# Optimization experiments

Hardware: AMD Instinct MI355X
Metric: run time of the kernel (lower is better)

Reference implementation:

```python
import jax
import jax.numpy as jnp
import numpy as np

N_NODES = 4096
N_EDGES = 65536
D_FEAT = 64


def setup_inputs() -> dict:
    key = jax.random.key(0)
    k1, k2, k3, k4 = jax.random.split(key, 4)
    x = jax.random.normal(k1, (N_NODES, D_FEAT), dtype=jnp.float32)
    edge_index = jax.random.randint(k2, (2, N_EDGES), 0, N_NODES, dtype=jnp.int32)
    batch = jnp.zeros((N_NODES,), dtype=jnp.int32)
    # GraphConv(in_channels, 1): lin_rel (with bias) on aggregated neighbors, lin_root on self
    w_rel = jax.random.normal(k3, (D_FEAT, 1), dtype=jnp.float32) * 0.1
    w_root = jax.random.normal(k4, (D_FEAT, 1), dtype=jnp.float32) * 0.1
    b = jnp.zeros((1,), dtype=jnp.float32)
    return {"x": x, "edge_index": edge_index, "batch": batch,
            "w_rel": w_rel, "w_root": w_root, "b": b}


def _merge_stars(x, src0, dst0, score):
    """Faithful sequential greedy star contraction (priority order by score desc)."""
    N = x.shape[0]
    order = jnp.argsort(-score)  # descending, ties like argsort

    def step(carry, node):
        xc, src, dst, remaining, center = carry
        active = remaining[node]
        # dests = set of targets of edges whose (current, rewritten) source == node,
        # minus already-chosen center nodes
        dest_edge = src == node                                  # [E]
        dest_node = jnp.zeros(N, bool).at[dst].max(dest_edge)    # node-level set
        dest_node = dest_node & ~center
        # torch does sum over list(dests)+[node]: node counted again (even on self-loop)
        combine = jnp.einsum('n,nd->d', dest_node.astype(xc.dtype), xc) + xc[node]
        D = dest_node.at[node].set(True)                         # dests U {node}
        x2 = xc.at[node].set(combine)
        src2 = jnp.where(D[src], node, src)                      # np.isin rewrite
        dst2 = jnp.where(D[dst], node, dst)
        rem2 = remaining & ~dest_node
        cen2 = center.at[node].set(True)
        carry2 = (jnp.where(active, x2, xc),
                  jnp.where(active, src2, src),
                  jnp.where(active, dst2, dst),
                  jnp.where(active, rem2, remaining),
                  jnp.where(active, cen2, center))
        return carry2, None

    init = (x, src0, dst0, jnp.ones(N, bool), jnp.zeros(N, bool))
    (x_final, _, _, remaining, _), _ = jax.lax.scan(step, init, order)
    return x_final, remaining


def reference(x, edge_index, batch, w_rel, w_root, b):
    N, d = x.shape
    src0, dst0 = edge_index[0], edge_index[1]
    # GraphConv score: W_rel * sum_{j->i} x_j + b + W_root * x_i ; dropout p=0; tanh
    agg = jax.ops.segment_sum(x[src0], dst0, num_segments=N)     # [N, d]
    score = jnp.tanh((agg @ w_rel + x @ w_root + b).reshape(-1)) # [N]

    x_final, remaining = _merge_stars(x, src0, dst0, score)

    # perm = sorted(nodes_remaining); outputs padded to static size N (sentinel -1)
    perm = jnp.nonzero(remaining, size=N, fill_value=N)[0]
    x_pooled = jnp.take(x_final, perm, axis=0, mode='fill', fill_value=0.0)
    kept = perm < N
    batch_pooled = jnp.where(kept, jnp.take(batch, jnp.minimum(perm, N - 1)), -1)
    # filter_adj on the ORIGINAL edge_index: keep edges with both endpoints kept,
    # relabel nodes to their rank among kept nodes; invalid edges -> -1
    relabel = jnp.cumsum(remaining.astype(jnp.int32)) - 1
    valid = remaining[src0] & remaining[dst0]
    new_src = jnp.where(valid, relabel[src0], -1)
    new_dst = jnp.where(valid, relabel[dst0], -1)
    new_edge_index = jnp.stack([new_src, new_dst])
    perm_out = jnp.where(kept, perm, -1)
    return x_pooled, new_edge_index, batch_pooled, perm_out
```

## Files before the change

### kernel.cpp

```cpp
#include <hip/hip_runtime.h>

#define NN 4096
#define NE 65536
#define ND 64


__global__ void k1_dots_count(const float* __restrict__ x, const float* __restrict__ wrel,
                              const float* __restrict__ wroot, const int* __restrict__ ei,
                              double* __restrict__ srel, double* __restrict__ sroot,
                              int* __restrict__ cnt) {
    int gt = blockIdx.x * blockDim.x + threadIdx.x;
    int node = gt >> 6, lane = gt & 63;
    double xv = (double)x[node * ND + lane];
    double pr = xv * (double)wrel[lane];
    double po = xv * (double)wroot[lane];
    for (int off = 32; off > 0; off >>= 1) {
        pr += __shfl_down(pr, off);
        po += __shfl_down(po, off);
    }
    if (lane == 0) {
        srel[node] = pr;
        sroot[node] = po;
    }
    if (gt < NE / 4) {
        const int4* eid4 = (const int4*)(ei + NE);
        int4 q = eid4[gt];
        atomicAdd(&cnt[q.x], 1);
        atomicAdd(&cnt[q.y], 1);
        atomicAdd(&cnt[q.z], 1);
        atomicAdd(&cnt[q.w], 1);
    }
}

__global__ void __launch_bounds__(1024) k2_scan(const int* __restrict__ cnt,
                                                int* __restrict__ rowst,
                                                int* __restrict__ cursor) {
    __shared__ int wt[16];
    int tid = threadIdx.x, lane = tid & 63, wv = tid >> 6;
    int4 c = ((const int4*)cnt)[tid];
    int tot = c.x + c.y + c.z + c.w;
    int inc = tot;
    for (int off = 1; off < 64; off <<= 1) {
        int v = __shfl_up(inc, off);
        if (lane >= off) inc += v;
    }
    if (lane == 63) wt[wv] = inc;
    __syncthreads();
    if (wv == 0 && lane < 16) {
        int v = wt[lane];
        for (int off = 1; off < 16; off <<= 1) {
            int u2 = __shfl_up(v, off);
            if (lane >= off) v += u2;
        }
        wt[lane] = v;
    }
    __syncthreads();
    int waveoff = (wv > 0) ? wt[wv - 1] : 0;
    int excl = waveoff + inc - tot;
    int4 rs;
    rs.x = excl; rs.y = excl + c.x; rs.z = excl + c.x + c.y; rs.w = excl + c.x + c.y + c.z;
    ((int4*)rowst)[tid] = rs;
    ((int4*)cursor)[tid] = rs;
    if (tid == 0) rowst[NN] = NE;
}

__global__ void k3_scatter(const int* __restrict__ ei, int* __restrict__ cursor,
                           unsigned short* __restrict__ incsr) {
    int i = blockIdx.x * blockDim.x + threadIdx.x;
    const int4* eis4 = (const int4*)ei;
    const int4* eid4 = (const int4*)(ei + NE);
    int4 s = eis4[i];
    int4 d = eid4[i];
    incsr[atomicAdd(&cursor[d.x], 1)] = (unsigned short)s.x;
    incsr[atomicAdd(&cursor[d.y], 1)] = (unsigned short)s.y;
    incsr[atomicAdd(&cursor[d.z], 1)] = (unsigned short)s.z;
    incsr[atomicAdd(&cursor[d.w], 1)] = (unsigned short)s.w;
}

__global__ void k4_keys(const double* __restrict__ srel, const double* __restrict__ sroot,
                        const float* __restrict__ bptr, const int* __restrict__ rowst,
                        const unsigned short* __restrict__ incsr, unsigned* __restrict__ key) {
    int v = blockIdx.x * blockDim.x + threadIdx.x;
    int rs = rowst[v], re = rowst[v + 1];
    double s = 0.0;
    for (int e = rs; e < re; ++e) s += srel[(int)incsr[e]];
    double arg = s + sroot[v] + (double)bptr[0];
    float sc = tanhf((float)arg);
    unsigned m = __float_as_uint(sc);
    m = (m & 0x80000000u) ? ~m : (m | 0x80000000u);
    key[v] = m;
}

__global__ void k5_filtersort(const int* __restrict__ rowst, const unsigned* __restrict__ key,
                              unsigned short* __restrict__ incsr, int* __restrict__ rl) {
    int gt = blockIdx.x * blockDim.x + threadIdx.x;
    int v = gt >> 6, l = gt & 63;
    int rs = rowst[v], deg = rowst[v + 1] - rs;
    unsigned mv = key[v];
    if (deg <= 64) {
        int u = (l < deg) ? (int)incsr[rs + l] : -1;
        bool isself = (l < deg) && (u == v);
        unsigned mu = (l < deg && !isself) ? key[u] : 0u;
        bool keep = (l < deg) && !isself && (mu > mv || (mu == mv && u < v));
        unsigned long long val = keep
            ? ((((unsigned long long)(~mu)) << 12) | (unsigned)u) : ~0ULL;
        int m = __popcll(__ballot(keep));
        bool selfAny = __ballot(isself) != 0ULL;
        for (int k = 2; k <= 64; k <<= 1) {
            for (int j = k >> 1; j > 0; j >>= 1) {
                unsigned long long o = __shfl_xor(val, j);
                bool takeMin = ((l & k) == 0) == ((l & j) == 0);
                unsigned long long mn = (o < val) ? o : val;
                unsigned long long mx = (o < val) ? val : o;
                val = takeMin ? mn : mx;
            }
        }
        if (l < m) incsr[rs + l] = (unsigned short)(val & 0xFFFULL);
        if (l == 0) rl[v] = m | (selfAny ? 0x10000 : 0);
    } else if (l == 0) {
        int w = rs;
        bool selfAny = false;
        for (int e = rs; e < rs + deg; ++e) {
            int u = (int)incsr[e];
            if (u == v) { selfAny = true; continue; }
            unsigned mu = key[u];
            if (!(mu > mv || (mu == mv && u < v))) continue;
            int j = w;
            while (j > rs) {
                int q = (int)incsr[j - 1];
                unsigned mq = key[q];
                if (mu > mq || (mu == mq && u < q)) { incsr[j] = (unsigned short)q; --j; }
                else break;
            }
            incsr[j] = (unsigned short)u; ++w;
        }
        rl[v] = (w - rs) | (selfAny ? 0x10000 : 0);
    }
}

__global__ void __launch_bounds__(1024) k34_fix(
        const int* __restrict__ rowst, const int* __restrict__ rl,
        const unsigned short* __restrict__ incsr_g,
        int* __restrict__ map_g, int* __restrict__ rem_g, int* __restrict__ relab_g,
        int* __restrict__ perm_a, int* __restrict__ nkeep_g) {
    __shared__ __align__(16) char buf[135232];
    unsigned short* incsr = (unsigned short*)buf;
    volatile unsigned char* stat = (volatile unsigned char*)(buf + 131072);
    int* wt = (int*)(buf + 135168);
    int tid = threadIdx.x, lane = tid & 63, wv = tid >> 6;

    for (int i = tid; i < 131072 / 16; i += 1024)
        ((int4*)incsr)[i] = ((const int4*)incsr_g)[i];
    ((int*)(buf + 131072))[tid] = 0;
    int4 rsq = ((const int4*)rowst)[tid];
    int4 rlq = ((const int4*)rl)[tid];
    int rs4[4] = {rsq.x, rsq.y, rsq.z, rsq.w};
    int rq4[4] = {rlq.x, rlq.y, rlq.z, rlq.w};
    __syncthreads();

    unsigned resolved = 0, centerm = 0, selfm = 0;
    int pos4[4], re4[4], fu4[4] = {0, 0, 0, 0};
    #pragma unroll
    for (int t = 0; t < 4; ++t) {
        int v = 4 * tid + t;
        int m = rq4[t] & 0xFFFF;
        if (rq4[t] & 0x10000) selfm |= 1u << t;
        int lo = rs4[t];
        pos4[t] = lo; re4[t] = lo + m;
        if (m == 0) {
            map_g[v] = v; stat[v] = 1;
            centerm |= 1u << t; resolved |= 1u << t;
        } else {
            fu4[t] = (int)incsr[lo];
        }
    }

    int guard = 0;
    while (resolved != 0xFu && guard < 1000000) {
        ++guard;
        bool prog = false;
        #pragma unroll
        for (int t = 0; t < 4; ++t) {
            if (resolved & (1u << t)) continue;
            int v = 4 * tid + t;
            int u = fu4[t];
            int st = (int)stat[u];
            if (st == 0) continue;
            prog = true;
            if (st == 1) {
                map_g[v] = u; stat[v] = 2; resolved |= 1u << t; continue;
            }
            int p = pos4[t] + 1, hi = re4[t];
            bool done = false;
            while (p < hi) {
                u = (int)incsr[p];
                st = (int)stat[u];
                if (st == 2) { ++p; continue; }
                if (st == 1) {
                    map_g[v] = u; stat[v] = 2; resolved |= 1u << t; done = true;
                }
                break;
            }
            if (!done) {
                if (p >= hi) {
                    map_g[v] = v; stat[v] = 1; centerm |= 1u << t; resolved |= 1u << t;
                } else {
                    pos4[t] = p; fu4[t] = u;
                }
            }
        }
        if (__ballot(prog) == 0) __builtin_amdgcn_s_sleep(1);
    }
    __syncthreads();

    int remb[4], cnt4 = 0;
    #pragma unroll
    for (int t = 0; t < 4; ++t) {
        remb[t] = ((centerm >> t) & 1) && !((selfm >> t) & 1);
        cnt4 += remb[t];
    }
    int inc2 = cnt4;
    for (int off = 1; off < 64; off <<= 1) {
        int v = __shfl_up(inc2, off);
        if (lane >= off) inc2 += v;
    }
    if (lane == 63) wt[wv] = inc2;
    __syncthreads();
    if (wv == 0 && lane < 16) {
        int v = wt[lane];
        for (int off = 1; off < 16; off <<= 1) {
            int u2 = __shfl_up(v, off);
            if (lane >= off) v += u2;
        }
        wt[lane] = v;
    }
    __syncthreads();
    int woff2 = (wv > 0) ? wt[wv - 1] : 0;
    int run = woff2 + inc2 - cnt4;
    #pragma unroll
    for (int t = 0; t < 4; ++t) {
        int v = 4 * tid + t;
        relab_g[v] = run;
        if (remb[t]) { perm_a[run] = v; ++run; }
        rem_g[v] = remb[t];
    }
    if (tid == 1023) nkeep_g[0] = run;
}

__global__ void k56_outputs(const float* __restrict__ x, const int* __restrict__ map_g,
                            const int* __restrict__ rem_g, const int* __restrict__ relab_g,
                            const int* __restrict__ perm_a, const int* __restrict__ ei,
                            const int* __restrict__ batch, const int* __restrict__ nkeep_g,
                            float* __restrict__ out) {
    int idx = blockIdx.x * blockDim.x + threadIdx.x;
    if (idx < NN * ND) {
        int n = idx >> 6, d = idx & 63;
        int m = map_g[n];
        if (rem_g[m]) atomicAdd(&out[relab_g[m] * ND + d], x[idx]);
    } else if (idx < NN * ND + 2 * NE) {
        int e = idx - NN * ND;
        int row = e >> 16;
        int ee = e & (NE - 1);
        int s = ei[ee], t = ei[NE + ee];
        bool valid = (rem_g[s] != 0) && (rem_g[t] != 0);
        int endp = (row == 0) ? s : t;
        out[idx] = valid ? (float)relab_g[endp] : -1.0f;
    } else if (idx < NN * ND + 2 * NE + NN) {
        int r = idx - (NN * ND + 2 * NE);
        int nk = nkeep_g[0];
        out[idx] = (r < nk) ? (float)batch[perm_a[r]] : -1.0f;
    } else if (idx < NN * ND + 2 * NE + 2 * NN) {
        int r = idx - (NN * ND + 2 * NE + NN);
        int nk = nkeep_g[0];
        out[idx] = (r < nk) ? (float)perm_a[r] : -1.0f;
    }
}

extern "C" void kernel_launch(void* const* d_in, const int* in_sizes, int n_in,
                              void* d_out, int out_size, void* d_ws, size_t ws_size,
                              hipStream_t stream) {
    const float* x     = (const float*)d_in[0];
    const int*   ei    = (const int*)d_in[1];
    const int*   batch = (const int*)d_in[2];
    const float* wrel  = (const float*)d_in[3];
    const float* wroot = (const float*)d_in[4];
    const float* b     = (const float*)d_in[5];

    char* ws = (char*)d_ws;
    double* srel   = (double*)(ws + 0);
    double* sroot  = (double*)(ws + 32768);
    int*    map_g  = (int*)(ws + 65536);
    int*    rem_g  = (int*)(ws + 81920);
    int*    relab  = (int*)(ws + 98304);
    int*    perma  = (int*)(ws + 114688);
    int*    nkeep  = (int*)(ws + 131072);
    int*    cnt    = (int*)(ws + 131136);
    int*    rowst  = (int*)(ws + 147520);
    int*    cursor = (int*)(ws + 163968);
    unsigned short* incsr = (unsigned short*)(ws + 180352);
    int*      rl  = cnt;
    unsigned* key = (unsigned*)cursor;

    float* out = (float*)d_out;

    hipMemsetAsync(out, 0, NN * ND * sizeof(float), stream);
    hipMemsetAsync(cnt, 0, NN * sizeof(int), stream);
    k1_dots_count<<<NN * ND / 256, 256, 0, stream>>>(x, wrel, wroot, ei, srel, sroot, cnt);
    k2_scan<<<1, 1024, 0, stream>>>(cnt, rowst, cursor);
    k3_scatter<<<(NE / 4) / 256, 256, 0, stream>>>(ei, cursor, incsr);
    k4_keys<<<NN / 256, 256, 0, stream>>>(srel, sroot, b, rowst, incsr, key);
    k5_filtersort<<<(NN * 64) / 256, 256, 0, stream>>>(rowst, key, incsr, rl);
    k34_fix<<<1, 1024, 0, stream>>>(rowst, rl, incsr, map_g, rem_g, relab, perma, nkeep);
    int total_out = NN * ND + 2 * NE + 2 * NN;
    k56_outputs<<<(total_out + 255) / 256, 256, 0, stream>>>(x, map_g, rem_g, relab,
                                                             perma, ei, batch, nkeep, out);
}
```

Baseline: 142.0 us.

## Fuse prefix scan into count kernel via last-block pattern; batch stat loads

```diff
diff --git a/kernel.cpp b/kernel.cpp
--- a/kernel.cpp
+++ b/kernel.cpp
@@ -5,13 +5,16 @@
 #define ND 64
 
 
-__global__ void k1_dots_count(const float* __restrict__ x, const float* __restrict__ wrel,
-                              const float* __restrict__ wroot, const int* __restrict__ ei,
-                              double* __restrict__ srel, double* __restrict__ sroot,
-                              int* __restrict__ cnt) {
+__global__ void k12_dots_count_scan(const float* __restrict__ x,
+                                    const float* __restrict__ wrel,
+                                    const float* __restrict__ wroot,
+                                    const int* __restrict__ ei,
+                                    double* __restrict__ srel, double* __restrict__ sroot,
+                                    int* __restrict__ cnt, int* __restrict__ done,
+                                    int* __restrict__ rowst, int* __restrict__ cursor) {
     int gt = blockIdx.x * blockDim.x + threadIdx.x;
     int node = gt >> 6, lane = gt & 63;
-    double xv = (double)x[node * ND + lane];
+    double xv = (double)x[gt];
     double pr = xv * (double)wrel[lane];
     double po = xv * (double)wroot[lane];
     for (int off = 32; off > 0; off >>= 1) {
@@ -30,38 +33,41 @@
         atomicAdd(&cnt[q.z], 1);
         atomicAdd(&cnt[q.w], 1);
     }
-}
-
-__global__ void __launch_bounds__(1024) k2_scan(const int* __restrict__ cnt,
-                                                int* __restrict__ rowst,
-                                                int* __restrict__ cursor) {
-    __shared__ int wt[16];
-    int tid = threadIdx.x, lane = tid & 63, wv = tid >> 6;
-    int4 c = ((const int4*)cnt)[tid];
-    int tot = c.x + c.y + c.z + c.w;
-    int inc = tot;
+    __threadfence();
+    __syncthreads();
+    __shared__ int isLast;
+    if (threadIdx.x == 0)
+        isLast = (atomicAdd(done, 1) == (int)gridDim.x - 1);
+    __syncthreads();
+    if (!isLast) return;
+
+    int tid = threadIdx.x;
+    int l2 = tid & 63, wv2 = tid >> 6;
+    __shared__ int wt2[4];
+    int vals[16], s = 0;
+    #pragma unroll
+    for (int k = 0; k < 16; ++k) {
+        vals[k] = __hip_atomic_load(&cnt[tid * 16 + k], __ATOMIC_RELAXED,
+                                    __HIP_MEMORY_SCOPE_AGENT);
+        s += vals[k];
+    }
+    int incl = s;
     for (int off = 1; off < 64; off <<= 1) {
-        int v = __shfl_up(inc, off);
-        if (lane >= off) inc += v;
-    }
-    if (lane == 63) wt[wv] = inc;
-    __syncthreads();
-    if (wv == 0 && lane < 16) {
-        int v = wt[lane];
-        for (int off = 1; off < 16; off <<= 1) {
-            int u2 = __shfl_up(v, off);
-            if (lane >= off) v += u2;
-        }
-        wt[lane] = v;
-    }
-    __syncthreads();
-    int waveoff = (wv > 0) ? wt[wv - 1] : 0;
-    int excl = waveoff + inc - tot;
-    int4 rs;
-    rs.x = excl; rs.y = excl + c.x; rs.z = excl + c.x + c.y; rs.w = excl + c.x + c.y + c.z;
-    ((int4*)rowst)[tid] = rs;
-    ((int4*)cursor)[tid] = rs;
-    if (tid == 0) rowst[NN] = NE;
+        int v = __shfl_up(incl, off);
+        if (l2 >= off) incl += v;
+    }
+    if (l2 == 63) wt2[wv2] = incl;
+    __syncthreads();
+    int woff = 0;
+    for (int w = 0; w < wv2; ++w) woff += wt2[w];
+    int run = woff + incl - s;
+    #pragma unroll
+    for (int k = 0; k < 16; ++k) {
+        rowst[tid * 16 + k] = run;
+        cursor[tid * 16 + k] = run;
+        run += vals[k];
+    }
+    if (tid == 255) rowst[NN] = NE;
 }
 
 __global__ void k3_scatter(const int* __restrict__ ei, int* __restrict__ cursor,
@@ -179,13 +185,16 @@
     while (resolved != 0xFu && guard < 1000000) {
         ++guard;
         bool prog = false;
+        int stq[4];
+        #pragma unroll
+        for (int t = 0; t < 4; ++t)
+            stq[t] = (resolved & (1u << t)) ? -1 : (int)stat[fu4[t]];
         #pragma unroll
         for (int t = 0; t < 4; ++t) {
-            if (resolved & (1u << t)) continue;
+            int st = stq[t];
+            if (st <= 0) continue;
             int v = 4 * tid + t;
             int u = fu4[t];
-            int st = (int)stat[u];
-            if (st == 0) continue;
             prog = true;
             if (st == 1) {
                 map_g[v] = u; stat[v] = 2; resolved |= 1u << t; continue;
@@ -294,6 +303,7 @@
     int*    relab  = (int*)(ws + 98304);
     int*    perma  = (int*)(ws + 114688);
     int*    nkeep  = (int*)(ws + 131072);
+    int*    done   = (int*)(ws + 131076);
     int*    cnt    = (int*)(ws + 131136);
     int*    rowst  = (int*)(ws + 147520);
     int*    cursor = (int*)(ws + 163968);
@@ -304,9 +314,9 @@
     float* out = (float*)d_out;
 
     hipMemsetAsync(out, 0, NN * ND * sizeof(float), stream);
-    hipMemsetAsync(cnt, 0, NN * sizeof(int), stream);
-    k1_dots_count<<<NN * ND / 256, 256, 0, stream>>>(x, wrel, wroot, ei, srel, sroot, cnt);
-    k2_scan<<<1, 1024, 0, stream>>>(cnt, rowst, cursor);
+    hipMemsetAsync(nkeep, 0, 16448, stream);
+    k12_dots_count_scan<<<NN * ND / 256, 256, 0, stream>>>(x, wrel, wroot, ei, srel,
+                                                           sroot, cnt, done, rowst, cursor);
     k3_scatter<<<(NE / 4) / 256, 256, 0, stream>>>(ei, cursor, incsr);
     k4_keys<<<NN / 256, 256, 0, stream>>>(srel, sroot, b, rowst, incsr, key);
     k5_filtersort<<<(NN * 64) / 256, 256, 0, stream>>>(rowst, key, incsr, rl);
```

Result: slower. 205.7 us (+44.9%).

## Resolve star contraction in priority-rank order with a single wave

Applied to the files above, without the earlier changes.

```diff
diff --git a/kernel.cpp b/kernel.cpp
--- a/kernel.cpp
+++ b/kernel.cpp
@@ -11,7 +11,7 @@
                               int* __restrict__ cnt) {
     int gt = blockIdx.x * blockDim.x + threadIdx.x;
     int node = gt >> 6, lane = gt & 63;
-    double xv = (double)x[node * ND + lane];
+    double xv = (double)x[gt];
     double pr = xv * (double)wrel[lane];
     double po = xv * (double)wroot[lane];
     for (int off = 32; off > 0; off >>= 1) {
@@ -92,9 +92,12 @@
 }
 
 __global__ void k5_filtersort(const int* __restrict__ rowst, const unsigned* __restrict__ key,
-                              unsigned short* __restrict__ incsr, int* __restrict__ rl) {
-    int gt = blockIdx.x * blockDim.x + threadIdx.x;
-    int v = gt >> 6, l = gt & 63;
+                              unsigned short* __restrict__ incsr, int* __restrict__ rl,
+                              int* __restrict__ r2n, float* __restrict__ out) {
+    int g = blockIdx.x * blockDim.x + threadIdx.x;
+    if (g < (NN * ND) / 4) ((float4*)out)[g] = make_float4(0.f, 0.f, 0.f, 0.f);
+
+    int v = g >> 6, l = g & 63;
     int rs = rowst[v], deg = rowst[v + 1] - rs;
     unsigned mv = key[v];
     if (deg <= 64) {
@@ -136,87 +139,87 @@
         }
         rl[v] = (w - rs) | (selfAny ? 0x10000 : 0);
     }
+
+    __shared__ unsigned kk[NN];
+    if (blockIdx.x < 16) {
+        for (int i = threadIdx.x; i < NN; i += 256) kk[i] = key[i];
+        __syncthreads();
+        int vv = (blockIdx.x << 8) | threadIdx.x;
+        unsigned kv = kk[vv];
+        int rank = 0;
+        for (int u4 = 0; u4 < NN; u4 += 4) {
+            unsigned a = kk[u4], b = kk[u4 + 1], c = kk[u4 + 2], d = kk[u4 + 3];
+            rank += (a > kv || (a == kv && (u4    ) < vv));
+            rank += (b > kv || (b == kv && (u4 + 1) < vv));
+            rank += (c > kv || (c == kv && (u4 + 2) < vv));
+            rank += (d > kv || (d == kv && (u4 + 3) < vv));
+        }
+        r2n[rank] = vv;
+    }
 }
 
 __global__ void __launch_bounds__(1024) k34_fix(
         const int* __restrict__ rowst, const int* __restrict__ rl,
-        const unsigned short* __restrict__ incsr_g,
+        const unsigned short* __restrict__ incsr_g, const int* __restrict__ r2n_g,
         int* __restrict__ map_g, int* __restrict__ rem_g, int* __restrict__ relab_g,
         int* __restrict__ perm_a, int* __restrict__ nkeep_g) {
-    __shared__ __align__(16) char buf[135232];
+    __shared__ __align__(16) char buf[155712];
     unsigned short* incsr = (unsigned short*)buf;
-    volatile unsigned char* stat = (volatile unsigned char*)(buf + 131072);
-    int* wt = (int*)(buf + 135168);
+    unsigned short* r2n   = (unsigned short*)(buf + 131072);
+    unsigned short* rst   = (unsigned short*)(buf + 139264);
+    unsigned char*  lsf   = (unsigned char*)(buf + 147456);
+    volatile unsigned char* stat = (volatile unsigned char*)(buf + 151552);
+    int* wt = (int*)(buf + 155648);
     int tid = threadIdx.x, lane = tid & 63, wv = tid >> 6;
 
-    for (int i = tid; i < 131072 / 16; i += 1024)
+    for (int i = tid; i < 8192; i += 1024)
         ((int4*)incsr)[i] = ((const int4*)incsr_g)[i];
-    ((int*)(buf + 131072))[tid] = 0;
-    int4 rsq = ((const int4*)rowst)[tid];
-    int4 rlq = ((const int4*)rl)[tid];
-    int rs4[4] = {rsq.x, rsq.y, rsq.z, rsq.w};
-    int rq4[4] = {rlq.x, rlq.y, rlq.z, rlq.w};
-    __syncthreads();
-
-    unsigned resolved = 0, centerm = 0, selfm = 0;
-    int pos4[4], re4[4], fu4[4] = {0, 0, 0, 0};
     #pragma unroll
     for (int t = 0; t < 4; ++t) {
-        int v = 4 * tid + t;
-        int m = rq4[t] & 0xFFFF;
-        if (rq4[t] & 0x10000) selfm |= 1u << t;
-        int lo = rs4[t];
-        pos4[t] = lo; re4[t] = lo + m;
-        if (m == 0) {
-            map_g[v] = v; stat[v] = 1;
-            centerm |= 1u << t; resolved |= 1u << t;
-        } else {
-            fu4[t] = (int)incsr[lo];
-        }
-    }
-
-    int guard = 0;
-    while (resolved != 0xFu && guard < 1000000) {
-        ++guard;
-        bool prog = false;
-        #pragma unroll
-        for (int t = 0; t < 4; ++t) {
-            if (resolved & (1u << t)) continue;
-            int v = 4 * tid + t;
-            int u = fu4[t];
-            int st = (int)stat[u];
-            if (st == 0) continue;
-            prog = true;
-            if (st == 1) {
-                map_g[v] = u; stat[v] = 2; resolved |= 1u << t; continue;
-            }
-            int p = pos4[t] + 1, hi = re4[t];
-            bool done = false;
-            while (p < hi) {
-                u = (int)incsr[p];
-                st = (int)stat[u];
-                if (st == 2) { ++p; continue; }
-                if (st == 1) {
-                    map_g[v] = u; stat[v] = 2; resolved |= 1u << t; done = true;
-                }
-                break;
-            }
-            if (!done) {
-                if (p >= hi) {
-                    map_g[v] = v; stat[v] = 1; centerm |= 1u << t; resolved |= 1u << t;
-                } else {
-                    pos4[t] = p; fu4[t] = u;
+        int v = (tid << 2) | t;
+        r2n[v] = (unsigned short)r2n_g[v];
+        rst[v] = (unsigned short)rowst[v];
+        int q = rl[v];
+        lsf[v] = (unsigned char)((q & 0x7F) | ((q & 0x10000) ? 0x80 : 0));
+        stat[v] = 0;
+    }
+    __syncthreads();
+
+    if (wv == 0) {
+        for (int c = 0; c < 64; ++c) {
+            int v = (int)r2n[(c << 6) | lane];
+            int len = lsf[v] & 0x7F;
+            int lo = (int)rst[v];
+            int p = 0;
+            bool undec = (len != 0);
+            if (!undec) { map_g[v] = v; stat[v] = 1; }
+            int rounds = 0;
+            while (__ballot(undec) != 0ULL && rounds < 200) {
+                ++rounds;
+                if (undec) {
+                    while (p < len) {
+                        int u = (int)incsr[lo + p];
+                        int st = (int)stat[u];
+                        if (st == 2) { ++p; continue; }
+                        if (st == 1) {
+                            map_g[v] = u; stat[v] = 2; undec = false;
+                        }
+                        break;
+                    }
+                    if (undec && p >= len) {
+                        map_g[v] = v; stat[v] = 1; undec = false;
+                    }
                 }
             }
         }
-        if (__ballot(prog) == 0) __builtin_amdgcn_s_sleep(1);
     }
     __syncthreads();
 
     int remb[4], cnt4 = 0;
     #pragma unroll
     for (int t = 0; t < 4; ++t) {
-        remb[t] = ((centerm >> t) & 1) && !((selfm >> t) & 1);
+        int v = (tid << 2) | t;
+        remb[t] = (stat[v] == 1) && !(lsf[v] & 0x80);
         cnt4 += remb[t];
     }
     int inc2 = cnt4;
@@ -239,7 +242,7 @@
     int run = woff2 + inc2 - cnt4;
     #pragma unroll
     for (int t = 0; t < 4; ++t) {
-        int v = 4 * tid + t;
+        int v = (tid << 2) | t;
         relab_g[v] = run;
         if (remb[t]) { perm_a[run] = v; ++run; }
         rem_g[v] = remb[t];
@@ -303,14 +306,14 @@
 
     float* out = (float*)d_out;
 
-    hipMemsetAsync(out, 0, NN * ND * sizeof(float), stream);
     hipMemsetAsync(cnt, 0, NN * sizeof(int), stream);
     k1_dots_count<<<NN * ND / 256, 256, 0, stream>>>(x, wrel, wroot, ei, srel, sroot, cnt);
     k2_scan<<<1, 1024, 0, stream>>>(cnt, rowst, cursor);
     k3_scatter<<<(NE / 4) / 256, 256, 0, stream>>>(ei, cursor, incsr);
     k4_keys<<<NN / 256, 256, 0, stream>>>(srel, sroot, b, rowst, incsr, key);
-    k5_filtersort<<<(NN * 64) / 256, 256, 0, stream>>>(rowst, key, incsr, rl);
-    k34_fix<<<1, 1024, 0, stream>>>(rowst, rl, incsr, map_g, rem_g, relab, perma, nkeep);
+    k5_filtersort<<<(NN * 64) / 256, 256, 0, stream>>>(rowst, key, incsr, rl, perma, out);
+    k34_fix<<<1, 1024, 0, stream>>>(rowst, rl, incsr, perma, map_g, rem_g, relab,
+                                    perma, nkeep);
     int total_out = NN * ND + 2 * NE + 2 * NN;
     k56_outputs<<<(total_out + 255) / 256, 256, 0, stream>>>(x, map_g, rem_g, relab,
                                                              perma, ei, batch, nkeep, out);
```

After: 390.7 us. 2.75x slower.
